# Kernel tuning notes

Hardware: AMD Instinct MI355X
Metric: run time of the kernel (lower is better)

## Reference

```python
import jax, jax.numpy as jnp
import numpy as np

N = 4096
F = 256
E = 65536
NEG = -1e30  # mask value for non-neighbors in distance top-k


def setup_inputs() -> dict:
    key = jax.random.key(0)
    k1, k2, k3, k4, k5 = jax.random.split(key, 5)
    edge_index = jax.random.randint(k1, (2, E), 0, N)
    edge_weight = jax.random.uniform(k2, (E,), dtype=jnp.float32)
    features = jax.random.normal(k3, (N, F), dtype=jnp.float32)
    theta_1 = jax.random.uniform(k4, (1,), dtype=jnp.float32)
    theta_2 = jax.random.uniform(k5, (1,), dtype=jnp.float32)
    return {"edge_index": edge_index, "edge_weight": edge_weight,
            "features": features, "theta_1": theta_1, "theta_2": theta_2}


def reference(edge_index, edge_weight, features, theta_1, theta_2):
    n = features.shape[0]
    row, col = edge_index[0], edge_index[1]
    # Adjacency construction is done on detached numpy in the original.
    w = jax.lax.stop_gradient(edge_weight)
    X = jax.lax.stop_gradient(features)
    # sp.csr_matrix sums duplicate (i,j) entries -> scatter-add; + I; clamp >1 to 1
    A = jnp.zeros((n, n), jnp.float32).at[row, col].add(w)
    A = A + jnp.eye(n, dtype=jnp.float32)
    A = jnp.where(A > 1.0, 1.0, A)
    A2 = A @ A  # adjs[1] = sp_A ** 2
    # generate_sparse_ids mutates both A and A_robust(=A2 for r=2) with setdiag(0)
    off = 1.0 - jnp.eye(n, dtype=jnp.float32)
    A = A * off
    A2 = A2 * off
    D = jnp.sum(A != 0.0, axis=1)    # per-node degree (count_nonzero)
    Dr = jnp.sum(A2 != 0.0, axis=1)  # robust (2-hop) degree
    Df = D.astype(jnp.float32)
    d_thres = jnp.mean(Df) + 2.0 * jnp.std(Df)  # euclidean metric branch
    # squared-euclidean distances via gram trick: ||xu - xv||^2
    sq = jnp.sum(X * X, axis=1)
    dist2 = sq[:, None] + sq[None, :] - 2.0 * (X @ X.T)
    nbr2 = A2 != 0.0  # A_robust neighbors (diag excluded, already zeroed)
    dmask = jnp.where(nbr2, dist2, NEG)
    # rank of each candidate in descending-distance order (stable argsort)
    order = jnp.argsort(-dmask, axis=1)
    rank = jnp.argsort(order, axis=1)
    # nz_sel = D_r[u] - round(sparse_rate * D[u]) with sparse_rate=2.0 (exact ints)
    nz_sel = Dr - 2 * D
    # faithful to numpy argsort()[-0:] which selects ALL neighbors when nz_sel==0
    nz_eff = jnp.where(nz_sel == 0, n, nz_sel)
    Z_sparse = nbr2 & (rank < nz_eff[:, None])  # top nz_sel farthest neighbors
    Z_high = A == 0.0  # highD branch: zero all non-1-hop-neighbors
    highD = Df > d_thres
    nosparse = (~highD) & (2 * D > Dr)  # empty sparse_ids branch
    Z = jnp.where(highD[:, None], Z_high,
                  jnp.where(nosparse[:, None], False, Z_sparse))
    adj_k = jnp.where(Z, 0.0, A2 - A)  # diag already zero in both
    vals = theta_1 * edge_weight + theta_2 * jax.lax.stop_gradient(adj_k[row, col])
    return jnp.clip(vals, 0.0, None)
```

## Files before the change

kernel.cpp:

```cpp
#include <hip/hip_runtime.h>

#define NN 4096
#define FF 256
#define EE 65536
#define MAXDEG 64
#define MAXEPR 256
#define NCAND 2048

__device__ __forceinline__ int wred_sum(int v) {
#pragma unroll
    for (int o = 32; o >= 1; o >>= 1) v += __shfl_xor(v, o);
    return v;
}

__global__ void k_scatter(const int* __restrict__ ei, int* __restrict__ ecnt,
                          int* __restrict__ elist) {
    int e = blockIdx.x * blockDim.x + threadIdx.x;
    if (e >= EE) return;
    int r = ei[e];
    int p = atomicAdd(&ecnt[r], 1);
    if (p < MAXEPR) elist[r * MAXEPR + p] = e;
}

__global__ void k_build(const int* __restrict__ ei, const float* __restrict__ ew,
                        const int* __restrict__ ecnt, const int* __restrict__ elist,
                        const float* __restrict__ X,
                        unsigned short* __restrict__ ccol, float* __restrict__ cval,
                        int* __restrict__ deg, double* __restrict__ sq) {
    __shared__ float row[NN];
    __shared__ int cnt;
    const int u = blockIdx.x;
    const int tid = threadIdx.x;
    const int lane = tid & 63;
    const unsigned long long lmask = (1ull << lane) - 1ull;

    for (int i = tid; i < NN; i += 256) row[i] = 0.f;
    if (tid == 0) cnt = 0;
    __syncthreads();

    int ne = ecnt[u]; if (ne > MAXEPR) ne = MAXEPR;
    for (int i = tid; i < ne; i += 256) {
        int e = elist[u * MAXEPR + i];
        int c = ei[EE + e];
        if (c != u) atomicAdd(&row[c], ew[e]);
    }
    __syncthreads();

    for (int i = tid; i < NN; i += 256) {
        float w = row[i];
        bool nzf = (w != 0.f);
        unsigned long long m = __ballot(nzf);
        int base = 0;
        if (lane == 0 && m) base = atomicAdd(&cnt, __popcll(m));
        base = __shfl(base, 0);
        int pos = base + __popcll(m & lmask);
        if (nzf && pos < MAXDEG) {
            ccol[u * MAXDEG + pos] = (unsigned short)i;
            cval[u * MAXDEG + pos] = fminf(w, 1.f);
        }
    }
    __syncthreads();
    if (tid == 0) deg[u] = cnt;

    if (tid < 64) {
        float4 x4 = ((const float4*)(X + (size_t)u * FF))[lane];
        double s = (double)x4.x * x4.x + (double)x4.y * x4.y +
                   (double)x4.z * x4.z + (double)x4.w * x4.w;
#pragma unroll
        for (int o = 32; o >= 1; o >>= 1) s += __shfl_xor(s, o);
        if (lane == 0) sq[u] = s;
    }
}

__global__ void k_stats(const int* __restrict__ deg, double* __restrict__ thres) {
    __shared__ double sd[256], sd2[256];
    int t = threadIdx.x;
    double s = 0, s2 = 0;
    for (int i = t; i < NN; i += 256) {
        double d = (double)deg[i];
        s += d; s2 += d * d;
    }
    sd[t] = s; sd2[t] = s2;
    __syncthreads();
    for (int o = 128; o >= 1; o >>= 1) {
        if (t < o) { sd[t] += sd[t + o]; sd2[t] += sd2[t + o]; }
        __syncthreads();
    }
    if (t == 0) {
        double mean = sd[0] / NN;
        double var = sd2[0] / NN - mean * mean;
        if (var < 0) var = 0;
        thres[0] = mean + 2.0 * sqrt(var);
    }
}

__launch_bounds__(256, 5)
__global__ void k_main(const int* __restrict__ ei, const float* __restrict__ ew,
                       const float* __restrict__ X, const float* __restrict__ th1p,
                       const float* __restrict__ th2p,
                       const unsigned short* __restrict__ ccol,
                       const float* __restrict__ cval, const int* __restrict__ deg,
                       const int* __restrict__ ecnt, const int* __restrict__ elist,
                       const double* __restrict__ sq, const double* __restrict__ thresp,
                       float* __restrict__ out) {
    __shared__ float acc[NN];
    __shared__ float Xu[FF];
    __shared__ unsigned short cidx[NCAND];
    __shared__ float cdist[NCAND];
    __shared__ unsigned short Aucol[MAXDEG];
    __shared__ float Auval[MAXDEG];
    __shared__ int ncand;

    const int u = blockIdx.x;
    const int tid = threadIdx.x;
    const int lane = tid & 63;
    const int wave = tid >> 6;
    const unsigned long long lmask = (1ull << lane) - 1ull;

    const int du = deg[u];
    const int dul = min(du, MAXDEG);
    for (int i = tid; i < NN; i += 256) acc[i] = 0.f;
    if (tid < FF / 4)
        ((float4*)Xu)[tid] = ((const float4*)(X + (size_t)u * FF))[tid];
    if (tid >= 128 && tid - 128 < dul) {
        Aucol[tid - 128] = ccol[u * MAXDEG + tid - 128];
        Auval[tid - 128] = cval[u * MAXDEG + tid - 128];
    }
    if (tid == 0) ncand = 0;
    __syncthreads();

    for (int kk = wave; kk <= dul; kk += 4) {
        int k; float wuk;
        if (kk == dul) { k = u; wuk = 1.f; }
        else { k = Aucol[kk]; wuk = Auval[kk]; }
        int dkl = min(deg[k], MAXDEG);
        for (int j = lane; j <= dkl; j += 64) {
            int v; float wkv;
            if (j == dkl) { v = k; wkv = 1.f; }
            else { v = ccol[k * MAXDEG + j]; wkv = cval[k * MAXDEG + j]; }
            atomicAdd(&acc[v], wuk * wkv);
        }
    }
    __syncthreads();
    if (tid == 0) acc[u] = 0.f;
    __syncthreads();

    for (int i = tid; i < NN; i += 256) {
        bool nzf = (acc[i] != 0.f);
        unsigned long long m = __ballot(nzf);
        int base = 0;
        if (lane == 0 && m) base = atomicAdd(&ncand, __popcll(m));
        base = __shfl(base, 0);
        int pos = base + __popcll(m & lmask);
        if (nzf && pos < NCAND) cidx[pos] = (unsigned short)i;
    }
    __syncthreads();
    const int Dr = ncand;
    const int Drs = min(Dr, NCAND);

    const double squ = sq[u];
    for (int c = tid; c < Drs; c += 256) {
        int v = cidx[c];
        const float4* __restrict__ Xv = (const float4*)(X + (size_t)v * FF);
        double sqv = sq[v];
        double s0 = 0, s1 = 0, s2 = 0, s3 = 0;
#pragma unroll 2
        for (int f = 0; f < FF / 4; f += 4) {
            float4 a0 = Xv[f + 0], a1 = Xv[f + 1], a2 = Xv[f + 2], a3 = Xv[f + 3];
            float4 b0 = ((const float4*)Xu)[f + 0];
            float4 b1 = ((const float4*)Xu)[f + 1];
            float4 b2 = ((const float4*)Xu)[f + 2];
            float4 b3 = ((const float4*)Xu)[f + 3];
            s0 += (double)a0.x * b0.x + (double)a0.y * b0.y +
                  (double)a0.z * b0.z + (double)a0.w * b0.w;
            s1 += (double)a1.x * b1.x + (double)a1.y * b1.y +
                  (double)a1.z * b1.z + (double)a1.w * b1.w;
            s2 += (double)a2.x * b2.x + (double)a2.y * b2.y +
                  (double)a2.z * b2.z + (double)a2.w * b2.w;
            s3 += (double)a3.x * b3.x + (double)a3.y * b3.y +
                  (double)a3.z * b3.z + (double)a3.w * b3.w;
        }
        cdist[c] = (float)(squ + sqv - 2.0 * (s0 + s1 + s2 + s3));
    }
    __syncthreads();

    const int D = du;
    const bool highD = ((double)D > thresp[0]);
    const int nz = Dr - 2 * D;
    const float th1 = th1p[0], th2 = th2p[0];
    int ne = ecnt[u]; if (ne > MAXEPR) ne = MAXEPR;
    for (int idx = wave; idx < ne; idx += 4) {
        int e = elist[u * MAXEPR + idx];
        int v = ei[EE + e];
        float w = ew[e];
        float a2v = acc[v];
        float avl = 0.f;
        bool hit = false;
        for (int t = lane; t < dul; t += 64)
            if ((int)Aucol[t] == v) { avl = Auval[t]; hit = true; }
        unsigned long long hm = __ballot(hit);
        float av = hm ? __shfl(avl, (int)__builtin_ctzll(hm)) : 0.f;
        float adj;
        if (highD) {
            adj = (av != 0.f) ? (a2v - av) : 0.f;
        } else if (nz < 0) {
            adj = a2v - av;
        } else if (nz == 0) {
            adj = 0.f;
        } else if (a2v == 0.f) {
            adj = 0.f;
        } else {
            float dvl = 0.f; bool fnd = false;
            for (int c = lane; c < Drs; c += 64)
                if ((int)cidx[c] == v) { dvl = cdist[c]; fnd = true; }
            unsigned long long fm = __ballot(fnd);
            float dv = __shfl(dvl, (int)__builtin_ctzll(fm));
            int cnt = 0;
            for (int c = lane; c < Drs; c += 64) {
                float cd = cdist[c];
                int ci = cidx[c];
                cnt += (cd > dv || (cd == dv && ci < v)) ? 1 : 0;
            }
            cnt = wred_sum(cnt);
            adj = (cnt < nz) ? 0.f : (a2v - av);
        }
        if (lane == 0) out[e] = fmaxf(0.f, fmaf(th1, w, th2 * adj));
    }
}

extern "C" void kernel_launch(void* const* d_in, const int* in_sizes, int n_in,
                              void* d_out, int out_size, void* d_ws, size_t ws_size,
                              hipStream_t stream) {
    const int* ei = (const int*)d_in[0];
    const float* ew = (const float*)d_in[1];
    const float* X = (const float*)d_in[2];
    const float* th1 = (const float*)d_in[3];
    const float* th2 = (const float*)d_in[4];
    float* out = (float*)d_out;

    char* ws = (char*)d_ws;
    size_t off = 0;
    unsigned short* ccol = (unsigned short*)(ws + off); off += (size_t)NN * MAXDEG * 2;
    float* cval = (float*)(ws + off);         off += (size_t)NN * MAXDEG * 4;
    int* deg = (int*)(ws + off);              off += (size_t)NN * 4;
    int* ecnt = (int*)(ws + off);             off += (size_t)NN * 4;
    double* sq = (double*)(ws + off);         off += (size_t)NN * 8;
    double* thres = (double*)(ws + off);      off += 256;
    int* elist = (int*)(ws + off);            off += (size_t)NN * MAXEPR * 4;

    hipMemsetAsync(ecnt, 0, (size_t)NN * 4, stream);

    k_scatter<<<EE / 256, 256, 0, stream>>>(ei, ecnt, elist);
    k_build<<<NN, 256, 0, stream>>>(ei, ew, ecnt, elist, X, ccol, cval, deg, sq);
    k_stats<<<1, 256, 0, stream>>>(deg, thres);
    k_main<<<NN, 256, 0, stream>>>(ei, ew, X, th1, th2, ccol, cval, deg,
                                   ecnt, elist, sq, thres, out);
}
```

Baseline: 277.5 us.

## Fuse degree stats into main kernel and compute distances wave-per-candidate

```diff
diff --git a/kernel.cpp b/kernel.cpp
--- a/kernel.cpp
+++ b/kernel.cpp
@@ -8,6 +8,11 @@
 #define NCAND 2048
 
 __device__ __forceinline__ int wred_sum(int v) {
+#pragma unroll
+    for (int o = 32; o >= 1; o >>= 1) v += __shfl_xor(v, o);
+    return v;
+}
+__device__ __forceinline__ double wred_dsum(double v) {
 #pragma unroll
     for (int o = 32; o >= 1; o >>= 1) v += __shfl_xor(v, o);
     return v;
@@ -34,7 +39,7 @@
     const int lane = tid & 63;
     const unsigned long long lmask = (1ull << lane) - 1ull;
 
-    for (int i = tid; i < NN; i += 256) row[i] = 0.f;
+    for (int i = tid; i < NN / 4; i += 256) ((float4*)row)[i] = make_float4(0.f, 0.f, 0.f, 0.f);
     if (tid == 0) cnt = 0;
     __syncthreads();
 
@@ -46,17 +51,21 @@
     }
     __syncthreads();
 
-    for (int i = tid; i < NN; i += 256) {
-        float w = row[i];
-        bool nzf = (w != 0.f);
-        unsigned long long m = __ballot(nzf);
-        int base = 0;
-        if (lane == 0 && m) base = atomicAdd(&cnt, __popcll(m));
-        base = __shfl(base, 0);
-        int pos = base + __popcll(m & lmask);
-        if (nzf && pos < MAXDEG) {
-            ccol[u * MAXDEG + pos] = (unsigned short)i;
-            cval[u * MAXDEG + pos] = fminf(w, 1.f);
+    for (int i4 = tid; i4 < NN / 4; i4 += 256) {
+        float4 a4 = ((float4*)row)[i4];
+        float e4[4] = {a4.x, a4.y, a4.z, a4.w};
+#pragma unroll
+        for (int j = 0; j < 4; ++j) {
+            bool nzf = (e4[j] != 0.f);
+            unsigned long long m = __ballot(nzf);
+            int base = 0;
+            if (lane == 0 && m) base = atomicAdd(&cnt, __popcll(m));
+            base = __shfl(base, 0);
+            int pos = base + __popcll(m & lmask);
+            if (nzf && pos < MAXDEG) {
+                ccol[u * MAXDEG + pos] = (unsigned short)(i4 * 4 + j);
+                cval[u * MAXDEG + pos] = fminf(e4[j], 1.f);
+            }
         }
     }
     __syncthreads();
@@ -66,31 +75,8 @@
         float4 x4 = ((const float4*)(X + (size_t)u * FF))[lane];
         double s = (double)x4.x * x4.x + (double)x4.y * x4.y +
                    (double)x4.z * x4.z + (double)x4.w * x4.w;
-#pragma unroll
-        for (int o = 32; o >= 1; o >>= 1) s += __shfl_xor(s, o);
+        s = wred_dsum(s);
         if (lane == 0) sq[u] = s;
-    }
-}
-
-__global__ void k_stats(const int* __restrict__ deg, double* __restrict__ thres) {
-    __shared__ double sd[256], sd2[256];
-    int t = threadIdx.x;
-    double s = 0, s2 = 0;
-    for (int i = t; i < NN; i += 256) {
-        double d = (double)deg[i];
-        s += d; s2 += d * d;
-    }
-    sd[t] = s; sd2[t] = s2;
-    __syncthreads();
-    for (int o = 128; o >= 1; o >>= 1) {
-        if (t < o) { sd[t] += sd[t + o]; sd2[t] += sd2[t + o]; }
-        __syncthreads();
-    }
-    if (t == 0) {
-        double mean = sd[0] / NN;
-        double var = sd2[0] / NN - mean * mean;
-        if (var < 0) var = 0;
-        thres[0] = mean + 2.0 * sqrt(var);
     }
 }
 
@@ -101,14 +87,15 @@
                        const unsigned short* __restrict__ ccol,
                        const float* __restrict__ cval, const int* __restrict__ deg,
                        const int* __restrict__ ecnt, const int* __restrict__ elist,
-                       const double* __restrict__ sq, const double* __restrict__ thresp,
-                       float* __restrict__ out) {
+                       const double* __restrict__ sq, float* __restrict__ out) {
     __shared__ float acc[NN];
     __shared__ float Xu[FF];
     __shared__ unsigned short cidx[NCAND];
     __shared__ float cdist[NCAND];
     __shared__ unsigned short Aucol[MAXDEG];
     __shared__ float Auval[MAXDEG];
+    __shared__ double sd[4], sd2[4];
+    __shared__ double thres_s;
     __shared__ int ncand;
 
     const int u = blockIdx.x;
@@ -119,7 +106,7 @@
 
     const int du = deg[u];
     const int dul = min(du, MAXDEG);
-    for (int i = tid; i < NN; i += 256) acc[i] = 0.f;
+    for (int i = tid; i < NN / 4; i += 256) ((float4*)acc)[i] = make_float4(0.f, 0.f, 0.f, 0.f);
     if (tid < FF / 4)
         ((float4*)Xu)[tid] = ((const float4*)(X + (size_t)u * FF))[tid];
     if (tid >= 128 && tid - 128 < dul) {
@@ -127,13 +114,35 @@
         Auval[tid - 128] = cval[u * MAXDEG + tid - 128];
     }
     if (tid == 0) ncand = 0;
-    __syncthreads();
-
+    {
+        double s = 0, s2 = 0;
+        for (int i = tid; i < NN; i += 256) {
+            double d = (double)deg[i];
+            s += d; s2 += d * d;
+        }
+        s = wred_dsum(s); s2 = wred_dsum(s2);
+        if (lane == 0) { sd[wave] = s; sd2[wave] = s2; }
+    }
+    __syncthreads();
+    if (tid == 0) {
+        double s = sd[0] + sd[1] + sd[2] + sd[3];
+        double s2 = sd2[0] + sd2[1] + sd2[2] + sd2[3];
+        double mean = s / NN;
+        double var = s2 / NN - mean * mean;
+        if (var < 0) var = 0;
+        thres_s = mean + 2.0 * sqrt(var);
+    }
+
+    int pcol = u; float pw = 1.f; int pdeg = dul;
+    if (lane < dul) {
+        pcol = Aucol[lane];
+        pw = Auval[lane];
+        pdeg = min(deg[pcol], MAXDEG);
+    }
     for (int kk = wave; kk <= dul; kk += 4) {
-        int k; float wuk;
-        if (kk == dul) { k = u; wuk = 1.f; }
-        else { k = Aucol[kk]; wuk = Auval[kk]; }
-        int dkl = min(deg[k], MAXDEG);
+        int k = (kk == dul) ? u : __shfl(pcol, kk);
+        float wuk = (kk == dul) ? 1.f : __shfl(pw, kk);
+        int dkl = (kk == dul) ? dul : __shfl(pdeg, kk);
         for (int j = lane; j <= dkl; j += 64) {
             int v; float wkv;
             if (j == dkl) { v = k; wkv = 1.f; }
@@ -145,47 +154,56 @@
     if (tid == 0) acc[u] = 0.f;
     __syncthreads();
 
-    for (int i = tid; i < NN; i += 256) {
-        bool nzf = (acc[i] != 0.f);
-        unsigned long long m = __ballot(nzf);
-        int base = 0;
-        if (lane == 0 && m) base = atomicAdd(&ncand, __popcll(m));
-        base = __shfl(base, 0);
-        int pos = base + __popcll(m & lmask);
-        if (nzf && pos < NCAND) cidx[pos] = (unsigned short)i;
+    for (int i4 = tid; i4 < NN / 4; i4 += 256) {
+        float4 a4 = ((float4*)acc)[i4];
+        float e4[4] = {a4.x, a4.y, a4.z, a4.w};
+#pragma unroll
+        for (int j = 0; j < 4; ++j) {
+            bool nzf = (e4[j] != 0.f);
+            unsigned long long m = __ballot(nzf);
+            int base = 0;
+            if (lane == 0 && m) base = atomicAdd(&ncand, __popcll(m));
+            base = __shfl(base, 0);
+            int pos = base + __popcll(m & lmask);
+            if (nzf && pos < NCAND) cidx[pos] = (unsigned short)(i4 * 4 + j);
+        }
     }
     __syncthreads();
     const int Dr = ncand;
     const int Drs = min(Dr, NCAND);
 
     const double squ = sq[u];
-    for (int c = tid; c < Drs; c += 256) {
-        int v = cidx[c];
-        const float4* __restrict__ Xv = (const float4*)(X + (size_t)v * FF);
-        double sqv = sq[v];
-        double s0 = 0, s1 = 0, s2 = 0, s3 = 0;
-#pragma unroll 2
-        for (int f = 0; f < FF / 4; f += 4) {
-            float4 a0 = Xv[f + 0], a1 = Xv[f + 1], a2 = Xv[f + 2], a3 = Xv[f + 3];
-            float4 b0 = ((const float4*)Xu)[f + 0];
-            float4 b1 = ((const float4*)Xu)[f + 1];
-            float4 b2 = ((const float4*)Xu)[f + 2];
-            float4 b3 = ((const float4*)Xu)[f + 3];
-            s0 += (double)a0.x * b0.x + (double)a0.y * b0.y +
-                  (double)a0.z * b0.z + (double)a0.w * b0.w;
-            s1 += (double)a1.x * b1.x + (double)a1.y * b1.y +
-                  (double)a1.z * b1.z + (double)a1.w * b1.w;
-            s2 += (double)a2.x * b2.x + (double)a2.y * b2.y +
-                  (double)a2.z * b2.z + (double)a2.w * b2.w;
-            s3 += (double)a3.x * b3.x + (double)a3.y * b3.y +
-                  (double)a3.z * b3.z + (double)a3.w * b3.w;
-        }
-        cdist[c] = (float)(squ + sqv - 2.0 * (s0 + s1 + s2 + s3));
+    const float4 b4 = ((const float4*)Xu)[lane];
+    for (int cb = wave * 8; cb < Drs; cb += 32) {
+        double sqv_l = 0.0;
+        if (lane < 8) {
+            int cl = cb + lane; cl = (cl < Drs) ? cl : (Drs - 1);
+            sqv_l = sq[cidx[cl]];
+        }
+        double d[8];
+#pragma unroll
+        for (int i = 0; i < 8; ++i) {
+            int ci = cb + i; ci = (ci < Drs) ? ci : (Drs - 1);
+            int v = cidx[ci];
+            float4 a = ((const float4*)(X + (size_t)v * FF))[lane];
+            d[i] = (double)a.x * b4.x + (double)a.y * b4.y +
+                   (double)a.z * b4.z + (double)a.w * b4.w;
+        }
+#pragma unroll
+        for (int i = 0; i < 8; ++i) {
+#pragma unroll
+            for (int o = 32; o >= 1; o >>= 1) d[i] += __shfl_xor(d[i], o);
+        }
+#pragma unroll
+        for (int i = 0; i < 8; ++i) {
+            if (lane == i && cb + i < Drs)
+                cdist[cb + i] = (float)(squ + sqv_l - 2.0 * d[i]);
+        }
     }
     __syncthreads();
 
     const int D = du;
-    const bool highD = ((double)D > thresp[0]);
+    const bool highD = ((double)D > thres_s);
     const int nz = Dr - 2 * D;
     const float th1 = th1p[0], th2 = th2p[0];
     int ne = ecnt[u]; if (ne > MAXEPR) ne = MAXEPR;
@@ -245,14 +263,12 @@
     int* deg = (int*)(ws + off);              off += (size_t)NN * 4;
     int* ecnt = (int*)(ws + off);             off += (size_t)NN * 4;
     double* sq = (double*)(ws + off);         off += (size_t)NN * 8;
-    double* thres = (double*)(ws + off);      off += 256;
     int* elist = (int*)(ws + off);            off += (size_t)NN * MAXEPR * 4;
 
     hipMemsetAsync(ecnt, 0, (size_t)NN * 4, stream);
 
     k_scatter<<<EE / 256, 256, 0, stream>>>(ei, ecnt, elist);
     k_build<<<NN, 256, 0, stream>>>(ei, ew, ecnt, elist, X, ccol, cval, deg, sq);
-    k_stats<<<1, 256, 0, stream>>>(deg, thres);
     k_main<<<NN, 256, 0, stream>>>(ei, ew, X, th1, th2, ccol, cval, deg,
-                                   ecnt, elist, sq, thres, out);
-}
+                                   ecnt, elist, sq, out);
+}
```

After: 296.4 us. +6.8%, slower.
